# Kernel tuning notes

Hardware: AMD Instinct MI355X
Metric: run time of the kernel (lower is better)

The kernel has to match this reference:

```python
import jax, jax.numpy as jnp
import numpy as np

NUM_CLASSES = 33  # labels 0..32; class 0 = background, 32 instances
EPS = 1e-06


def _lovasz_hinge_flat(logits, labels):
    # logits, labels: flat 1-D float arrays (labels in {0,1})
    signs = 2.0 * labels - 1.0
    errors = 1.0 - logits * signs
    order = jnp.argsort(-errors)            # descending sort
    errors_sorted = errors[order]
    gt_sorted = labels[order]
    gts = jnp.sum(gt_sorted)
    intersection = gts - jnp.cumsum(gt_sorted)
    union = gts + jnp.cumsum(1.0 - gt_sorted)
    jaccard = 1.0 - intersection / union
    grad = jnp.concatenate([jaccard[:1], jaccard[1:] - jaccard[:-1]])
    return jnp.dot(jax.nn.relu(errors_sorted), grad)


def _per_sample_loss(y_emb, y_sig, gt_patch):
    # y_emb: [2,H,W] float, y_sig: [1,H,W] float, gt_patch: [1,H,W] int
    # to_onehot(gt)[0, 1:] -> [N,H,W], N = NUM_CLASSES-1 instance channels
    gt_one_hot = jax.nn.one_hot(gt_patch[0], NUM_CLASSES, axis=0, dtype=y_emb.dtype)[1:]
    counts = jnp.sum(gt_one_hot, axis=(1, 2), keepdims=True)          # [N,1,1]
    # per-instance embedding centers: [2,N,1,1]
    centers = jnp.sum(gt_one_hot[None] * y_emb[:, None], axis=(2, 3), keepdims=True) / counts
    instance_sigmas = gt_one_hot[None] * y_sig[:, None]               # [1,N,H,W]
    sigmas = jnp.sum(instance_sigmas, axis=(2, 3), keepdims=True) / counts  # [1,N,1,1]
    var_sigmas = jnp.sum(((instance_sigmas - jax.lax.stop_gradient(sigmas)) * gt_one_hot) ** 2) / counts  # [N,1,1]
    center_dist = jnp.linalg.norm(centers - y_emb[:, None], axis=0)   # [N,H,W]
    probs = jnp.exp(-0.5 * (center_dist / sigmas) ** 2)               # [1,N,H,W]
    logits = (probs * 2.0 - 1.0).reshape(-1)
    labels = jnp.broadcast_to(gt_one_hot[None], probs.shape).reshape(-1)
    return _lovasz_hinge_flat(logits, labels) + jnp.mean(var_sigmas)


def setup_inputs() -> dict:
    key = jax.random.key(0)
    k1, k2, k3 = jax.random.split(key, 3)
    B, H, W = 4, 512, 512
    y_embeddings = jax.random.normal(k1, (B, 2, H, W), dtype=jnp.float32)
    y_sigma = jax.random.uniform(k2, (B, 1, H, W), dtype=jnp.float32)
    y_true = jax.random.randint(k3, (B, 1, H, W), 0, NUM_CLASSES, dtype=jnp.int64)
    return {"y_embeddings": y_embeddings, "y_sigma": y_sigma, "y_true": y_true}


def reference(y_embeddings, y_sigma, y_true):
    # Assumes every sample contains foreground (random labels over 512x512
    # guarantee this w.h.p.), so the torch `if torch.any(gt>0)` branch is taken
    # for all samples and the final loss is the mean over the batch.
    losses = jax.vmap(_per_sample_loss)(y_embeddings, y_sigma, y_true)
    return jnp.mean(losses)
```

## Files before the change

kernel.cpp:

```cpp
#include <hip/hip_runtime.h>

#define HW    262144
#define BNUM  4
#define NC    33
#define NI    32

#define NB     1024
#define BSCALE 64.0f
#define EG     4096
#define ESCALE 2048.0f

typedef unsigned long long ull;

#define W_CNTB 8192
#define W_CNTF 8196
#define W_FINL 8200
#define W_PART 8208
#define PJ 168
#define PS (128 * PJ)

__global__ void __launch_bounds__(256) stats_kernel(
    const float* __restrict__ emb, const float* __restrict__ sig,
    const int* __restrict__ gt, float* __restrict__ ws) {
  int s = blockIdx.y;
  int j = blockIdx.x;
  int t = threadIdx.x;
  int w = t >> 6;
  __shared__ float acc[4][165];
  int bid = s * 128 + j;
  unsigned* wsu = (unsigned*)ws;
  if (t < 16) {
    wsu[bid * 16 + t] = 0u;
    if (bid == 0) wsu[8192 + t] = 0u;
  }
  for (int k = t; k < 4 * 165; k += 256) ((float*)acc)[k] = 0.f;
  __syncthreads();
  const float* e0p = emb + (size_t)s * 2 * HW;
  const float* e1p = e0p + HW;
  const float* sp  = sig + (size_t)s * HW;
  const int*   gp  = gt  + (size_t)s * HW;
  #pragma unroll
  for (int i = 0; i < 2; ++i) {
    int idx = j * 2048 + i * 1024 + t * 4;
    int4   lb = *(const int4*)(gp + idx);
    float4 x  = *(const float4*)(e0p + idx);
    float4 y  = *(const float4*)(e1p + idx);
    float4 sg = *(const float4*)(sp + idx);
#define ACC(L, X, Y, SG)                                                   \
    if (L > 0) {                                                           \
      atomicAdd(&acc[w][L], X);        atomicAdd(&acc[w][33 + L], Y);      \
      atomicAdd(&acc[w][66 + L], SG);  atomicAdd(&acc[w][99 + L], (SG)*(SG)); \
      atomicAdd(&acc[w][132 + L], 1.0f);                                   \
    }
    ACC(lb.x, x.x, y.x, sg.x)
    ACC(lb.y, x.y, y.y, sg.y)
    ACC(lb.z, x.z, y.z, sg.z)
    ACC(lb.w, x.w, y.w, sg.w)
#undef ACC
  }
  __syncthreads();
  if (t < 165) {
    float v = acc[0][t] + acc[1][t] + acc[2][t] + acc[3][t];
    ws[W_PART + s * PS + j * PJ + t] = v;
  }
}

__global__ void __launch_bounds__(512) hist_scan_kernel(
    const float* __restrict__ emb, const int* __restrict__ gt,
    float* __restrict__ ws, float* __restrict__ out) {
  int s  = blockIdx.y;
  int lb = blockIdx.x;
  __shared__ unsigned hist[EG * 2];
  __shared__ float sums[165];
  __shared__ float4 cons[NC];
  __shared__ ull wsum[8];
  __shared__ float red[8];
  __shared__ float vart_s;
  __shared__ int flag;
  int t = threadIdx.x;
  int lane = t & 63, wid = t >> 6;
  for (int k = t; k < NB * 4; k += 512) hist[k] = 0u;
  if (t < 165) {
    const float* pp = ws + W_PART + s * PS + t;
    float sum = 0.f;
    #pragma unroll 8
    for (int j = 0; j < 128; ++j) sum += pp[j * PJ];
    sums[t] = sum;
  }
  __syncthreads();
  if (t >= 1 && t < NC) {
    float c = sums[132 + t];
    float4 C;
    if (c > 0.f) {
      float inv = 1.0f / c;
      float c0 = sums[t] * inv, c1 = sums[33 + t] * inv, sgm = sums[66 + t] * inv;
      float Q = 0.5f / (sgm * sgm) * BSCALE;
      C.x = Q; C.y = -2.0f * Q * c0; C.z = -2.0f * Q * c1;
      C.w = Q * (c0 * c0 + c1 * c1);
    } else {
      C.x = 0.f; C.y = 0.f; C.z = 0.f; C.w = (float)NB;
    }
    cons[t] = C;
  }
  __syncthreads();
  const float* e0p = emb + (size_t)s * 2 * HW;
  const float* e1p = e0p + HW;
  const int*   gp  = gt  + (size_t)s * HW;
  int idx = lb * 2048 + t * 4;
  int4   lbl = *(const int4*)(gp + idx);
  float4 px  = *(const float4*)(e0p + idx);
  float4 py  = *(const float4*)(e1p + idx);
  float4 ss;
  ss.x = fmaf(px.x, px.x, py.x * py.x);
  ss.y = fmaf(px.y, px.y, py.y * py.y);
  ss.z = fmaf(px.z, px.z, py.z * py.z);
  ss.w = fmaf(px.w, px.w, py.w * py.w);
  unsigned* hr = hist + (t & 3);
  #pragma unroll 4
  for (int n = 1; n <= NI; ++n) {
    float4 C = cons[n];
#define ITEM(P0, P1, SV, L)                                            \
    {                                                                  \
      float bf = fmaf(C.x, SV, fmaf(C.y, P0, fmaf(C.z, P1, C.w)));     \
      int ib = (int)bf;                                                \
      bool pos = (L == n);                                             \
      if (pos) ib = min(ib, NB - 1);                                   \
      if (ib < NB) atomicAdd(&hr[ib << 2], pos ? 0x10000u : 1u);       \
    }
    ITEM(px.x, py.x, ss.x, lbl.x)
    ITEM(px.y, py.y, ss.y, lbl.y)
    ITEM(px.z, py.z, ss.z, lbl.z)
    ITEM(px.w, py.w, ss.w, lbl.w)
#undef ITEM
  }
  __syncthreads();
  ull* th = ((ull*)ws) + (size_t)s * NB;
  for (int k = t; k < NB; k += 512) {
    unsigned v = hist[k*4] + hist[k*4+1] + hist[k*4+2] + hist[k*4+3];
    if (v) {
      ull add = ((ull)(v >> 16) << 32) | (v & 0xFFFFu);
      atomicAdd(&th[k], add);
    }
  }
  __syncthreads();
  if (t == 0) {
    __threadfence();
    flag = (atomicAdd((unsigned*)ws + W_CNTB + s, 1u) == 127u);
  }
  __syncthreads();
  if (!flag) return;

  unsigned* ep = hist;
  unsigned* en = hist + EG;
  for (int k = t; k < 2 * EG; k += 512) hist[k] = 0u;
  if (wid == 0) {
    float S = 0.f, rcp = 0.f;
    if (lane >= 1 && lane < NC) {
      float c = sums[132 + lane];
      if (c > 0.f) {
        float sg = sums[66 + lane] / c;
        S = sums[99 + lane] - c * sg * sg;
        rcp = 1.0f / c;
      }
    }
    for (int o = 32; o; o >>= 1) {
      S   += __shfl_down(S, o);
      rcp += __shfl_down(rcp, o);
    }
    if (lane == 0) vart_s = S * rcp / (float)NI;
  }
  __syncthreads();
  for (int b = t; b < NB; b += 512) {
    ull v = atomicAdd(&th[b], 0ull);
    unsigned pos = (unsigned)(v >> 32), neg = (unsigned)(v & 0xFFFFFFFFu);
    if (pos | neg) {
      float tc = ((float)b + 0.5f) * (1.0f / BSCALE);
      float ex = __expf(-tc);
      if (pos) {
        float e = 2.0f - 2.0f * ex;
        int k = (int)(e * ESCALE); if (k > EG - 1) k = EG - 1;
        atomicAdd(&ep[k], pos);
      }
      if (neg) {
        float e = 2.0f * ex;
        int k = (int)(e * ESCALE); if (k > EG - 1) k = EG - 1;
        atomicAdd(&en[k], neg);
      }
    }
  }
  __syncthreads();
  const int CH = EG / 512;
  int j0 = t * CH;
  unsigned np = 0, nn = 0;
  for (int k = 0; k < CH; ++k) {
    int b = EG - 1 - (j0 + k);
    np += ep[b]; nn += en[b];
  }
  ull v = ((ull)np << 32) | (ull)nn;
  ull inc = v;
  for (int o = 1; o < 64; o <<= 1) {
    ull u = __shfl_up(inc, o);
    if (lane >= o) inc += u;
  }
  if (lane == 63) wsum[wid] = inc;
  __syncthreads();
  ull offset = 0, total = 0;
  for (int i = 0; i < 8; ++i) {
    ull xr = wsum[i];
    if (i < wid) offset += xr;
    total += xr;
  }
  ull excl = offset + inc - v;
  float P = (float)(unsigned)(total >> 32);
  unsigned p = (unsigned)(excl >> 32), f = (unsigned)(excl & 0xFFFFFFFFu);
  float jprev = 1.0f - (P - (float)p) / (P + (float)f);
  float contrib = 0.f;
  for (int k = 0; k < CH; ++k) {
    int b = EG - 1 - (j0 + k);
    unsigned ap_ = ep[b], an_ = en[b];
    if (ap_ | an_) {
      p += ap_; f += an_;
      float j = 1.0f - (P - (float)p) / (P + (float)f);
      float e = ((float)b + 0.5f) * (2.0f / EG);
      contrib += e * (j - jprev);
      jprev = j;
    }
  }
  for (int o = 32; o; o >>= 1) contrib += __shfl_down(contrib, o);
  if (lane == 0) red[wid] = contrib;
  __syncthreads();
  if (t == 0) {
    float tot = 0.f;
    for (int i = 0; i < 8; ++i) tot += red[i];
    float loss = tot + vart_s;
    float* fin = ws + W_FINL;
    atomicExch(&fin[s], loss);
    __threadfence();
    unsigned old = atomicAdd((unsigned*)ws + W_CNTF, 1u);
    if (old == BNUM - 1) {
      float a = 0.f;
      for (int i = 0; i < BNUM; ++i) a += atomicAdd(&fin[i], 0.0f);
      out[0] = a * (1.0f / BNUM);
    }
  }
}

extern "C" void kernel_launch(void* const* d_in, const int* in_sizes, int n_in,
                              void* d_out, int out_size, void* d_ws, size_t ws_size,
                              hipStream_t stream) {
  const float* emb = (const float*)d_in[0];
  const float* sig = (const float*)d_in[1];
  const int*   gt  = (const int*)d_in[2];
  float* out = (float*)d_out;
  float* ws  = (float*)d_ws;

  dim3 gA(128, BNUM);
  stats_kernel<<<gA, 256, 0, stream>>>(emb, sig, gt, ws);
  dim3 gB(128, BNUM);
  hist_scan_kernel<<<gB, 512, 0, stream>>>(emb, gt, ws, out);
}
```

Baseline: 116.7 us.

## Replace global 64-bit histogram atomics with per-block partial histograms and simplify the inner loop

Each block now writes its full 1024-bin partial histogram to its own workspace slot with plain stores. The last block per sample reduces all 128 partials, which removes contended global 64-bit atomics. The per-instance inner loop also drops its label-compare branch: every pixel is counted as negative in all classes, then a separate pre-pass adds 0xFFFF to the pixel's own-class bin, which through 16-bit wraparound turns that count into a positive. The cost is a larger workspace footprint and a serial 128-way reduction in the final block, and it relies on the 16-bit packed fields wrapping correctly.

```diff
diff --git a/kernel.cpp b/kernel.cpp
--- a/kernel.cpp
+++ b/kernel.cpp
@@ -12,10 +12,11 @@
 
 typedef unsigned long long ull;
 
-#define W_CNTB 8192
-#define W_CNTF 8196
-#define W_FINL 8200
-#define W_PART 8208
+#define W_CNTB 0
+#define W_CNTF 4
+#define W_FINL 8
+#define W_HIST 16
+#define W_PART (W_HIST + BNUM * 128 * NB)
 #define PJ 168
 #define PS (128 * PJ)
 
@@ -29,10 +30,7 @@
   __shared__ float acc[4][165];
   int bid = s * 128 + j;
   unsigned* wsu = (unsigned*)ws;
-  if (t < 16) {
-    wsu[bid * 16 + t] = 0u;
-    if (bid == 0) wsu[8192 + t] = 0u;
-  }
+  if (bid == 0 && t < 16) wsu[t] = 0u;
   for (int k = t; k < 4 * 165; k += 256) ((float*)acc)[k] = 0.f;
   __syncthreads();
   const float* e0p = emb + (size_t)s * 2 * HW;
@@ -116,36 +114,44 @@
   ss.z = fmaf(px.z, px.z, py.z * py.z);
   ss.w = fmaf(px.w, px.w, py.w * py.w);
   unsigned* hr = hist + (t & 3);
+#define POSFIX(P0, P1, SV, L)                                            \
+    if (L > 0) {                                                         \
+      float4 C = cons[L];                                                \
+      float bf = fmaf(C.x, SV, fmaf(C.y, P0, fmaf(C.z, P1, C.w)));       \
+      int ib = min((int)bf, NB - 1);                                     \
+      atomicAdd(&hr[ib << 2], 0xFFFFu);                                  \
+    }
+  POSFIX(px.x, py.x, ss.x, lbl.x)
+  POSFIX(px.y, py.y, ss.y, lbl.y)
+  POSFIX(px.z, py.z, ss.z, lbl.z)
+  POSFIX(px.w, py.w, ss.w, lbl.w)
+#undef POSFIX
   #pragma unroll 4
   for (int n = 1; n <= NI; ++n) {
     float4 C = cons[n];
-#define ITEM(P0, P1, SV, L)                                            \
+#define ITEM(P0, P1, SV)                                               \
     {                                                                  \
       float bf = fmaf(C.x, SV, fmaf(C.y, P0, fmaf(C.z, P1, C.w)));     \
-      int ib = (int)bf;                                                \
-      bool pos = (L == n);                                             \
-      if (pos) ib = min(ib, NB - 1);                                   \
-      if (ib < NB) atomicAdd(&hr[ib << 2], pos ? 0x10000u : 1u);       \
-    }
-    ITEM(px.x, py.x, ss.x, lbl.x)
-    ITEM(px.y, py.y, ss.y, lbl.y)
-    ITEM(px.z, py.z, ss.z, lbl.z)
-    ITEM(px.w, py.w, ss.w, lbl.w)
+      int ib = min((int)bf, NB - 1);                                   \
+      atomicAdd(&hr[ib << 2], 1u);                                     \
+    }
+    ITEM(px.x, py.x, ss.x)
+    ITEM(px.y, py.y, ss.y)
+    ITEM(px.z, py.z, ss.z)
+    ITEM(px.w, py.w, ss.w)
 #undef ITEM
   }
   __syncthreads();
-  ull* th = ((ull*)ws) + (size_t)s * NB;
+  unsigned* gh = (unsigned*)ws + W_HIST + (s * 128 + lb) * NB;
   for (int k = t; k < NB; k += 512) {
-    unsigned v = hist[k*4] + hist[k*4+1] + hist[k*4+2] + hist[k*4+3];
-    if (v) {
-      ull add = ((ull)(v >> 16) << 32) | (v & 0xFFFFu);
-      atomicAdd(&th[k], add);
-    }
+    unsigned v = hist[k * 4] + hist[k * 4 + 1] + hist[k * 4 + 2] + hist[k * 4 + 3];
+    __hip_atomic_store(&gh[k], v, __ATOMIC_RELAXED, __HIP_MEMORY_SCOPE_AGENT);
   }
   __syncthreads();
   if (t == 0) {
     __threadfence();
-    flag = (atomicAdd((unsigned*)ws + W_CNTB + s, 1u) == 127u);
+    flag = (__hip_atomic_fetch_add((unsigned*)ws + W_CNTB + s, 1u,
+              __ATOMIC_ACQ_REL, __HIP_MEMORY_SCOPE_AGENT) == 127u);
   }
   __syncthreads();
   if (!flag) return;
@@ -170,9 +176,16 @@
     if (lane == 0) vart_s = S * rcp / (float)NI;
   }
   __syncthreads();
+  unsigned* ghs = (unsigned*)ws + W_HIST + s * 128 * NB;
   for (int b = t; b < NB; b += 512) {
-    ull v = atomicAdd(&th[b], 0ull);
-    unsigned pos = (unsigned)(v >> 32), neg = (unsigned)(v & 0xFFFFFFFFu);
+    unsigned pos = 0, neg = 0;
+    #pragma unroll 16
+    for (int j = 0; j < 128; ++j) {
+      unsigned v = __hip_atomic_load(&ghs[j * NB + b],
+                     __ATOMIC_RELAXED, __HIP_MEMORY_SCOPE_AGENT);
+      pos += v >> 16;
+      neg += v & 0xFFFFu;
+    }
     if (pos | neg) {
       float tc = ((float)b + 0.5f) * (1.0f / BSCALE);
       float ex = __expf(-tc);
```

Measured after the change: 133.2 us. +14.1%, slower.

## Split center computation into its own kernel and widen histogram sub-copies

Applied to the files above, without the earlier changes.

The per-sample reduction of partial statistics and the Gaussian constants move out of every histogram block into a small separate kernel that writes them to workspace. Each of the 512 histogram blocks no longer repeats the 128-way partial sum. The histogram now uses 8 interleaved sub-copies instead of 4 to reduce shared-atomic contention. The positive-label case is handled by one pre-pass adding 0xFFFF, so the 32-class loop always does an unconditional atomic. This costs an extra kernel launch and makes every out-of-range bin clamp to the last bin instead of being skipped.

```diff
diff --git a/kernel.cpp b/kernel.cpp
--- a/kernel.cpp
+++ b/kernel.cpp
@@ -15,7 +15,9 @@
 #define W_CNTB 8192
 #define W_CNTF 8196
 #define W_FINL 8200
-#define W_PART 8208
+#define W_VART 8204
+#define W_CONS 8208
+#define W_PART 8736
 #define PJ 168
 #define PS (128 * PJ)
 
@@ -65,28 +67,23 @@
   }
 }
 
-__global__ void __launch_bounds__(512) hist_scan_kernel(
-    const float* __restrict__ emb, const int* __restrict__ gt,
-    float* __restrict__ ws, float* __restrict__ out) {
-  int s  = blockIdx.y;
-  int lb = blockIdx.x;
-  __shared__ unsigned hist[EG * 2];
-  __shared__ float sums[165];
-  __shared__ float4 cons[NC];
-  __shared__ ull wsum[8];
-  __shared__ float red[8];
-  __shared__ float vart_s;
-  __shared__ int flag;
+__global__ void __launch_bounds__(512) cons_kernel(float* __restrict__ ws) {
+  int s = blockIdx.x;
   int t = threadIdx.x;
   int lane = t & 63, wid = t >> 6;
-  for (int k = t; k < NB * 4; k += 512) hist[k] = 0u;
-  if (t < 165) {
-    const float* pp = ws + W_PART + s * PS + t;
+  __shared__ float sums2[2][165];
+  __shared__ float sums[165];
+  if (t < 330) {
+    int r = (t >= 165) ? 1 : 0;
+    int c = t - r * 165;
+    const float* pp = ws + W_PART + s * PS + (r << 6) * PJ + c;
     float sum = 0.f;
-    #pragma unroll 8
-    for (int j = 0; j < 128; ++j) sum += pp[j * PJ];
-    sums[t] = sum;
-  }
+    #pragma unroll 16
+    for (int jj = 0; jj < 64; ++jj) sum += pp[jj * PJ];
+    sums2[r][c] = sum;
+  }
+  __syncthreads();
+  if (t < 165) sums[t] = sums2[0][t] + sums2[1][t];
   __syncthreads();
   if (t >= 1 && t < NC) {
     float c = sums[132 + t];
@@ -100,8 +97,40 @@
     } else {
       C.x = 0.f; C.y = 0.f; C.z = 0.f; C.w = (float)NB;
     }
-    cons[t] = C;
-  }
+    ((float4*)(ws + W_CONS))[s * NC + t] = C;
+  }
+  if (wid == 0) {
+    float S = 0.f, rcp = 0.f;
+    if (lane >= 1 && lane < NC) {
+      float c = sums[132 + lane];
+      if (c > 0.f) {
+        float sg = sums[66 + lane] / c;
+        S = sums[99 + lane] - c * sg * sg;
+        rcp = 1.0f / c;
+      }
+    }
+    for (int o = 32; o; o >>= 1) {
+      S   += __shfl_down(S, o);
+      rcp += __shfl_down(rcp, o);
+    }
+    if (lane == 0) ws[W_VART + s] = S * rcp / (float)NI;
+  }
+}
+
+__global__ void __launch_bounds__(512) hist_scan_kernel(
+    const float* __restrict__ emb, const int* __restrict__ gt,
+    float* __restrict__ ws, float* __restrict__ out) {
+  int s  = blockIdx.y;
+  int lb = blockIdx.x;
+  __shared__ unsigned hist[NB * 8];
+  __shared__ float4 cons[NC];
+  __shared__ ull wsum[8];
+  __shared__ float red[8];
+  __shared__ int flag;
+  int t = threadIdx.x;
+  int lane = t & 63, wid = t >> 6;
+  for (int k = t; k < NB * 8; k += 512) hist[k] = 0u;
+  if (t < NC) cons[t] = ((const float4*)(ws + W_CONS))[s * NC + t];
   __syncthreads();
   const float* e0p = emb + (size_t)s * 2 * HW;
   const float* e1p = e0p + HW;
@@ -115,28 +144,40 @@
   ss.y = fmaf(px.y, px.y, py.y * py.y);
   ss.z = fmaf(px.z, px.z, py.z * py.z);
   ss.w = fmaf(px.w, px.w, py.w * py.w);
-  unsigned* hr = hist + (t & 3);
+  unsigned* hr = hist + (t & 7);
+#define POSFIX(P0, P1, SV, L)                                            \
+    if (L > 0) {                                                         \
+      float4 C = cons[L];                                                \
+      float bf = fmaf(C.x, SV, fmaf(C.y, P0, fmaf(C.z, P1, C.w)));       \
+      int ib = min((int)bf, NB - 1);                                     \
+      atomicAdd(&hr[ib << 3], 0xFFFFu);                                  \
+    }
+  POSFIX(px.x, py.x, ss.x, lbl.x)
+  POSFIX(px.y, py.y, ss.y, lbl.y)
+  POSFIX(px.z, py.z, ss.z, lbl.z)
+  POSFIX(px.w, py.w, ss.w, lbl.w)
+#undef POSFIX
   #pragma unroll 4
   for (int n = 1; n <= NI; ++n) {
     float4 C = cons[n];
-#define ITEM(P0, P1, SV, L)                                            \
+#define ITEM(P0, P1, SV)                                               \
     {                                                                  \
       float bf = fmaf(C.x, SV, fmaf(C.y, P0, fmaf(C.z, P1, C.w)));     \
-      int ib = (int)bf;                                                \
-      bool pos = (L == n);                                             \
-      if (pos) ib = min(ib, NB - 1);                                   \
-      if (ib < NB) atomicAdd(&hr[ib << 2], pos ? 0x10000u : 1u);       \
-    }
-    ITEM(px.x, py.x, ss.x, lbl.x)
-    ITEM(px.y, py.y, ss.y, lbl.y)
-    ITEM(px.z, py.z, ss.z, lbl.z)
-    ITEM(px.w, py.w, ss.w, lbl.w)
+      int ib = min((int)bf, NB - 1);                                   \
+      atomicAdd(&hr[ib << 3], 1u);                                     \
+    }
+    ITEM(px.x, py.x, ss.x)
+    ITEM(px.y, py.y, ss.y)
+    ITEM(px.z, py.z, ss.z)
+    ITEM(px.w, py.w, ss.w)
 #undef ITEM
   }
   __syncthreads();
   ull* th = ((ull*)ws) + (size_t)s * NB;
   for (int k = t; k < NB; k += 512) {
-    unsigned v = hist[k*4] + hist[k*4+1] + hist[k*4+2] + hist[k*4+3];
+    uint4 a = *(uint4*)&hist[k * 8];
+    uint4 b = *(uint4*)&hist[k * 8 + 4];
+    unsigned v = a.x + a.y + a.z + a.w + b.x + b.y + b.z + b.w;
     if (v) {
       ull add = ((ull)(v >> 16) << 32) | (v & 0xFFFFu);
       atomicAdd(&th[k], add);
@@ -153,22 +194,7 @@
   unsigned* ep = hist;
   unsigned* en = hist + EG;
   for (int k = t; k < 2 * EG; k += 512) hist[k] = 0u;
-  if (wid == 0) {
-    float S = 0.f, rcp = 0.f;
-    if (lane >= 1 && lane < NC) {
-      float c = sums[132 + lane];
-      if (c > 0.f) {
-        float sg = sums[66 + lane] / c;
-        S = sums[99 + lane] - c * sg * sg;
-        rcp = 1.0f / c;
-      }
-    }
-    for (int o = 32; o; o >>= 1) {
-      S   += __shfl_down(S, o);
-      rcp += __shfl_down(rcp, o);
-    }
-    if (lane == 0) vart_s = S * rcp / (float)NI;
-  }
+  float vart = ws[W_VART + s];
   __syncthreads();
   for (int b = t; b < NB; b += 512) {
     ull v = atomicAdd(&th[b], 0ull);
@@ -232,7 +258,7 @@
   if (t == 0) {
     float tot = 0.f;
     for (int i = 0; i < 8; ++i) tot += red[i];
-    float loss = tot + vart_s;
+    float loss = tot + vart;
     float* fin = ws + W_FINL;
     atomicExch(&fin[s], loss);
     __threadfence();
@@ -256,6 +282,7 @@
 
   dim3 gA(128, BNUM);
   stats_kernel<<<gA, 256, 0, stream>>>(emb, sig, gt, ws);
+  cons_kernel<<<BNUM, 512, 0, stream>>>(ws);
   dim3 gB(128, BNUM);
   hist_scan_kernel<<<gB, 512, 0, stream>>>(emb, gt, ws, out);
 }
```

Measured after the change: 114.8 us. Within noise of the previous version (-1.6%).
